# Performance work log

Hardware: AMD Instinct MI355X
Metric: run time of the kernel (lower is better)

The kernel has to match this reference:

```python
import jax, jax.numpy as jnp
import numpy as np
import math

B, S, D, H = 1, 2048, 4096, 32
HD = D // H  # 128
BASE = 10000.0
NEG = -1e9


def rotate_half(x):
    x1, x2 = x[..., : x.shape[-1] // 2], x[..., x.shape[-1] // 2 :]
    return jnp.concatenate((-x2, x1), axis=-1)


def setup_inputs() -> dict:
    key = jax.random.key(0)
    ks = jax.random.split(key, 5)
    scale = 1.0 / math.sqrt(D)
    hidden_states = jax.random.normal(ks[0], (B, S, D), dtype=jnp.float32)
    Wq = jax.random.normal(ks[1], (D, D), dtype=jnp.float32) * scale
    Wk = jax.random.normal(ks[2], (D, D), dtype=jnp.float32) * scale
    Wv = jax.random.normal(ks[3], (D, D), dtype=jnp.float32) * scale
    Wo = jax.random.normal(ks[4], (D, D), dtype=jnp.float32) * scale
    # causal additive mask [1,1,S,S]
    causal = jnp.tril(jnp.ones((S, S), dtype=bool))
    attention_mask = jnp.where(causal, 0.0, NEG).astype(jnp.float32)[None, None]
    # rotary cos/sin cache [1,1,S,HD]
    inv_freq = 1.0 / (BASE ** (jnp.arange(0, HD, 2, dtype=jnp.float32) / HD))
    freqs = jnp.arange(S, dtype=jnp.float32)[:, None] * inv_freq[None, :]
    emb = jnp.concatenate((freqs, freqs), axis=-1)
    cos = jnp.cos(emb)[None, None]
    sin = jnp.sin(emb)[None, None]
    return dict(hidden_states=hidden_states, attention_mask=attention_mask,
                cos=cos, sin=sin, Wq=Wq, Wk=Wk, Wv=Wv, Wo=Wo)


def reference(hidden_states, attention_mask, cos, sin, Wq, Wk, Wv, Wo):
    b, s, d = hidden_states.shape
    # projections (torch Linear: x @ W.T), reshape to [B,H,S,HD]
    def proj(W):
        return (hidden_states @ W.T).reshape(b, s, H, HD).transpose(0, 2, 1, 3)
    q, k, v = proj(Wq), proj(Wk), proj(Wv)
    # RoPE
    q = q * cos + rotate_half(q) * sin
    k = k * cos + rotate_half(k) * sin
    # scores [B,H,S,S], key pre-scaled as in original
    scores = jnp.einsum('bhqd,bhkd->bhqk', q, k / math.sqrt(HD)) + attention_mask
    attn = jax.nn.softmax(scores.astype(jnp.float32), axis=-1).astype(scores.dtype)
    out = jnp.einsum('bhqk,bhkd->bhqd', attn, v)
    out = out.transpose(0, 2, 1, 3).reshape(b, s, d)
    return out @ Wo.T
```

## Files before the change

### kernel.cpp

```cpp
#include <hip/hip_runtime.h>
#include <hip/hip_bf16.h>
#include <stdint.h>

#define DEV __device__ __forceinline__

typedef __bf16 bf16x8 __attribute__((ext_vector_type(8)));
typedef float f32x4 __attribute__((ext_vector_type(4)));
typedef unsigned short ushort8_t __attribute__((ext_vector_type(8)));
typedef unsigned short ushort4_t __attribute__((ext_vector_type(4)));

constexpr int S = 2048;
constexpr int D = 4096;
constexpr int H = 32;
constexpr int HD = 128;
constexpr float kSc = 0.08838834764831845f * 1.4426950408889634f;

DEV unsigned short f2bf(float f) {
    uint32_t u = __builtin_bit_cast(uint32_t, f);
    u += 0x7fffu + ((u >> 16) & 1u);
    return (unsigned short)(u >> 16);
}
DEV float bf2f(unsigned short h) {
    uint32_t u = ((uint32_t)h) << 16;
    return __builtin_bit_cast(float, u);
}

DEV void gload_lds16(const void* g, void* l) {
    __builtin_amdgcn_global_load_lds(
        (const __attribute__((address_space(1))) void*)g,
        (__attribute__((address_space(3))) void*)l,
        16, 0, 0);
}

DEV f32x4 mfma16(bf16x8 a, bf16x8 b, f32x4 c) {
    return __builtin_amdgcn_mfma_f32_16x16x32_bf16(a, b, c, 0, 0, 0);
}

__global__ __launch_bounds__(256) void cvt_all(const float* __restrict__ hs,
                                               const float* __restrict__ w0,
                                               const float* __restrict__ w1,
                                               const float* __restrict__ w2,
                                               const float* __restrict__ w3,
                                               unsigned short* __restrict__ hsb,
                                               unsigned short* __restrict__ o0,
                                               unsigned short* __restrict__ o1,
                                               unsigned short* __restrict__ o2,
                                               unsigned short* __restrict__ o3) {
    const int b = blockIdx.x;
    const float* in;
    unsigned short* out;
    size_t blk;
    if (b < 4096) {
        in = hs; out = hsb; blk = (size_t)b;
    } else {
        const int i = b - 4096;
        const int w = i >> 13;
        const int r = i & 8191;
        in  = (w == 0) ? w0 : (w == 1) ? w1 : (w == 2) ? w2 : w3;
        out = (w == 0) ? o0 : (w == 1) ? o1 : (w == 2) ? o2 : o3;
        blk = (size_t)r;
    }
    const size_t i8 = blk * 256 + threadIdx.x;
    f32x4 a = ((const f32x4*)in)[2 * i8];
    f32x4 c = ((const f32x4*)in)[2 * i8 + 1];
    ushort8_t o;
    o[0] = f2bf(a[0]); o[1] = f2bf(a[1]); o[2] = f2bf(a[2]); o[3] = f2bf(a[3]);
    o[4] = f2bf(c[0]); o[5] = f2bf(c[1]); o[6] = f2bf(c[2]); o[7] = f2bf(c[3]);
    ((ushort8_t*)out)[i8] = o;
}

__global__ __launch_bounds__(512, 2) void gemm_qkv8(const unsigned short* __restrict__ Ap,
                                                    const unsigned short* __restrict__ wq,
                                                    const unsigned short* __restrict__ wk,
                                                    const unsigned short* __restrict__ wv,
                                                    unsigned short* __restrict__ Qb,
                                                    unsigned short* __restrict__ Kb,
                                                    unsigned short* __restrict__ Vt) {
    extern __shared__ unsigned short lds8[];
    unsigned short (*As)[8192] = (unsigned short(*)[8192])lds8;
    unsigned short (*Bs)[8192] = (unsigned short(*)[8192])(lds8 + 32768);

    const int tix = threadIdx.x;
    const int lane = tix & 63;
    const int w = tix >> 6;
    const int g = (lane >> 4);
    const int rl = lane & 15;
    const int wm = w >> 2;
    const int wn = w & 3;
    const int bh = wn >> 1;
    const int bc0 = (wn & 1) * 64;
    const int rx = rl & 7;

    const int bid = blockIdx.x;
    const int wg = (bid & 7) * 48 + (bid >> 3);
    const int xx = wg % 48;
    const int yy = wg / 48;
    const int m0 = yy * 256;
    const int n0g = xx * 256;
    const int wsel = n0g >> 12;
    const int n0 = n0g & 4095;
    const unsigned short* Bp = (wsel == 0) ? wq : (wsel == 1) ? wk : wv;

    int srow[2], scol[2];
#pragma unroll
    for (int u = 0; u < 2; ++u) {
        const int c = u * 512 + tix;
        srow[u] = c >> 3;
        scol[u] = (((c & 7) ^ (srow[u] & 7)) << 3);
    }

    const char* aBase[2] = {(const char*)As[wm], (const char*)As[2 + wm]};
    const char* bBase[2] = {(const char*)Bs[bh], (const char*)Bs[2 + bh]};

    f32x4 acc[4][2][4] = {};
    bf16x8 bfr[4][2];

#define STG_A(kt, h, slot)                                                        \
    if ((kt) < 64) {                                                              \
        _Pragma("unroll") for (int u = 0; u < 2; ++u)                             \
            gload_lds16(Ap + (size_t)(m0 + (h) * 128 + srow[u]) * 4096 +          \
                            (kt) * 64 + scol[u],                                  \
                        &As[slot][(u * 512 + tix) * 8]);                          \
    }
#define STG_B(kt, h, slot)                                                        \
    if ((kt) < 64) {                                                              \
        _Pragma("unroll") for (int u = 0; u < 2; ++u)                             \
            gload_lds16(Bp + (size_t)(n0 + (h) * 128 + srow[u]) * 4096 +          \
                            (kt) * 64 + scol[u],                                  \
                        &Bs[slot][(u * 512 + tix) * 8]);                          \
    }

#define PHASE(pt, q, STG, VM)                                                     \
    {                                                                             \
        bf16x8 af[2][2];                                                          \
        _Pragma("unroll") for (int mi = 0; mi < 2; ++mi)                          \
        _Pragma("unroll") for (int ks = 0; ks < 2; ++ks) {                        \
            const int ab = ((q) * 32 + mi * 16 + rl) * 128 +                      \
                           ((((ks << 2) + g) ^ rx) << 4);                         \
            af[mi][ks] = *(const bf16x8*)(aBase[pt] + ab);                        \
        }                                                                         \
        if ((q) == 0) {                                                           \
            _Pragma("unroll") for (int nt = 0; nt < 4; ++nt)                      \
            _Pragma("unroll") for (int ks = 0; ks < 2; ++ks) {                    \
                const int bb = (bc0 + nt * 16 + rl) * 128 +                       \
                               ((((ks << 2) + g) ^ rx) << 4);                     \
                bfr[nt][ks] = *(const bf16x8*)(bBase[pt] + bb);                   \
            }                                                                     \
        }                                                                         \
        STG;                                                                      \
        if (VM) asm volatile("s_waitcnt vmcnt(4)" ::: "memory");                  \
        __builtin_amdgcn_s_barrier();                                             \
        __builtin_amdgcn_s_setprio(1);                                            \
        _Pragma("unroll") for (int ks = 0; ks < 2; ++ks)                          \
        _Pragma("unroll") for (int mi = 0; mi < 2; ++mi)                          \
        _Pragma("unroll") for (int nt = 0; nt < 4; ++nt)                          \
            acc[q][mi][nt] = mfma16(af[mi][ks], bfr[nt][ks], acc[q][mi][nt]);     \
        __builtin_amdgcn_s_setprio(0);                                            \
        __builtin_amdgcn_s_barrier();                                             \
    }

    STG_A(0, 0, 0); STG_A(0, 1, 1);
    STG_B(0, 0, 0); STG_B(0, 1, 1);
    STG_B(1, 0, 2); STG_B(1, 1, 3);
    __syncthreads();

    for (int i = 0; i < 32; ++i) {
        const int o = 2 * i + 1, ne = 2 * i + 2, no = 2 * i + 3;
        PHASE(0, 0, STG_A(o, 0, 2), 0)
        PHASE(0, 1, STG_A(o, 1, 3), 0)
        PHASE(0, 2, STG_B(ne, 0, 0), 0)
        PHASE(0, 3, STG_B(ne, 1, 1), 1)
        PHASE(1, 0, STG_A(ne, 0, 0), 0)
        PHASE(1, 1, STG_A(ne, 1, 1), 0)
        PHASE(1, 2, STG_B(no, 0, 2), 0)
        PHASE(1, 3, STG_B(no, 1, 3), 1)
    }
#undef PHASE
#undef STG_A
#undef STG_B

#pragma unroll
    for (int q = 0; q < 4; ++q)
#pragma unroll
        for (int mi = 0; mi < 2; ++mi)
#pragma unroll
            for (int nt = 0; nt < 4; ++nt) {
                const int row0 = m0 + wm * 128 + q * 32 + mi * 16 + g * 4;
                const int colg = n0 + wn * 64 + nt * 16 + rl;
                if (wsel == 2) {
                    ushort4_t v;
#pragma unroll
                    for (int r = 0; r < 4; ++r) v[r] = f2bf(acc[q][mi][nt][r]);
                    *(ushort4_t*)&Vt[(size_t)colg * S + row0] = v;
                } else {
                    unsigned short* o = (wsel == 0) ? Qb : Kb;
#pragma unroll
                    for (int r = 0; r < 4; ++r)
                        o[(size_t)(row0 + r) * 4096 + colg] = f2bf(acc[q][mi][nt][r]);
                }
            }
}

__global__ __launch_bounds__(256) void gemm_out(const unsigned short* __restrict__ A,
                                                const unsigned short* __restrict__ B,
                                                float* __restrict__ C) {
    __shared__ unsigned short As[128 * 64];
    __shared__ unsigned short Bs[128 * 64];
    const int t = threadIdx.x;
    const int lane = t & 63;
    const int wid = t >> 6;
    const int g = lane >> 4;
    const int rl = lane & 15;

    const int bid = blockIdx.x;
    const int wg = (bid & 7) * 64 + (bid >> 3);
    const int xx = wg % 32;
    const int yy = wg / 32;
    const int m0 = yy * 128;
    const int n0 = xx * 128;

    const int wm = (wid >> 1) * 64;
    const int wn = (wid & 1) * 64;
    constexpr int K = D, N = D;

    f32x4 acc[4][4] = {};

    for (int kt = 0; kt < K; kt += 64) {
#pragma unroll
        for (int r = 0; r < 4; ++r) {
            const int c = r * 256 + t;
            const int row = c >> 3;
            const int src = (c & 7) ^ (row & 7);
            const int dstChunk = r * 256 + wid * 64;
            gload_lds16(A + (size_t)(m0 + row) * K + kt + src * 8, &As[dstChunk * 8]);
            gload_lds16(B + (size_t)(n0 + row) * K + kt + src * 8, &Bs[dstChunk * 8]);
        }
        __syncthreads();
#pragma unroll
        for (int ks = 0; ks < 2; ++ks) {
            bf16x8 af[4], bfv[4];
#pragma unroll
            for (int i = 0; i < 4; ++i) {
                const int rowa = wm + i * 16 + rl;
                af[i] = *(const bf16x8*)&As[rowa * 64 + (((ks * 4 + g) ^ (rowa & 7)) << 3)];
                const int rowb = wn + i * 16 + rl;
                bfv[i] = *(const bf16x8*)&Bs[rowb * 64 + (((ks * 4 + g) ^ (rowb & 7)) << 3)];
            }
#pragma unroll
            for (int mi = 0; mi < 4; ++mi)
#pragma unroll
                for (int ni = 0; ni < 4; ++ni)
                    acc[mi][ni] = mfma16(af[mi], bfv[ni], acc[mi][ni]);
        }
        __syncthreads();
    }

#pragma unroll
    for (int mi = 0; mi < 4; ++mi) {
#pragma unroll
        for (int ni = 0; ni < 4; ++ni) {
            const int grow = m0 + wm + mi * 16 + g * 4;
            const int gcol = n0 + wn + ni * 16 + rl;
#pragma unroll
            for (int r = 0; r < 4; ++r)
                C[(size_t)(grow + r) * N + gcol] = acc[mi][ni][r];
        }
    }
}

__global__ __launch_bounds__(256) void rope_kernel(unsigned short* __restrict__ Qb,
                                                   unsigned short* __restrict__ Kb,
                                                   const float* __restrict__ cosT,
                                                   const float* __restrict__ sinT) {
    const int i = blockIdx.x * 256 + threadIdx.x;
    const int j8 = i & 7;
    const int h = (i >> 3) & 31;
    const int s = i >> 8;
    const size_t base = (size_t)s * D + h * HD + j8 * 8;
    const float* cp = cosT + s * HD + j8 * 8;
    const float* sp = sinT + s * HD + j8 * 8;
    float c1[8], s1[8], c2[8], s2[8];
#pragma unroll
    for (int k = 0; k < 8; ++k) { c1[k] = cp[k]; s1[k] = sp[k]; c2[k] = cp[k + 64]; s2[k] = sp[k + 64]; }

#pragma unroll
    for (int w = 0; w < 2; ++w) {
        unsigned short* p = (w == 0 ? Qb : Kb) + base;
        const float f = (w == 0) ? kSc : 1.0f;
        ushort8_t x1 = *(ushort8_t*)p;
        ushort8_t x2 = *(ushort8_t*)(p + 64);
        ushort8_t o1, o2;
#pragma unroll
        for (int k = 0; k < 8; ++k) {
            const float a = bf2f(x1[k]);
            const float b = bf2f(x2[k]);
            o1[k] = f2bf((a * c1[k] - b * s1[k]) * f);
            o2[k] = f2bf((b * c2[k] + a * s2[k]) * f);
        }
        *(ushort8_t*)p = o1;
        *(ushort8_t*)(p + 64) = o2;
    }
}

constexpr int NQT = S / 128;
__global__ __launch_bounds__(256, 2) void flash_attn(const unsigned short* __restrict__ Q,
                                                     const unsigned short* __restrict__ K,
                                                     const unsigned short* __restrict__ V,
                                                     unsigned short* __restrict__ O) {
    __shared__ unsigned short Ks[2][64 * 128];
    __shared__ unsigned short Vs[128 * 64];
    __shared__ unsigned short Ps[4][32 * 64];

    const int t = threadIdx.x;
    const int lane = t & 63;
    const int wid = t >> 6;
    const int g = lane >> 4;
    const int rl = lane & 15;
    const int bid = blockIdx.x;
    const int qt = (NQT - 1) - (bid >> 5);
    const int h = bid & 31;
    const int q0 = qt * 128;
    const int wrow0 = q0 + wid * 32;

    bf16x8 qf[2][4];
#pragma unroll
    for (int mi = 0; mi < 2; ++mi) {
        const unsigned short* qp = Q + (size_t)(wrow0 + mi * 16 + rl) * D + h * HD;
#pragma unroll
        for (int ks = 0; ks < 4; ++ks) qf[mi][ks] = *(const bf16x8*)(qp + ks * 32 + g * 8);
    }

    f32x4 accO[2][8] = {};
    float m2s[2] = {-1e30f, -1e30f};
    float lsum[2] = {0.f, 0.f};

#pragma unroll
    for (int r = 0; r < 4; ++r) {
        const int c = r * 256 + t;
        const int rowk = c >> 4;
        const int srck = (c & 15) ^ (rowk & 7);
        gload_lds16(K + (size_t)rowk * D + h * HD + srck * 8,
                    &Ks[0][(r * 256 + wid * 64) * 8]);
    }
    __syncthreads();

    int cur = 0;
    const int ntiles = 2 * qt + 2;
    for (int kv = 0; kv < ntiles; ++kv) {
        const int kv0 = kv * 64;
#pragma unroll
        for (int r = 0; r < 4; ++r) {
            const int c = r * 256 + t;
            const int rowv = c >> 3;
            const int srcv = (c & 7) ^ (rowv & 7);
            gload_lds16(V + (size_t)(h * HD + rowv) * S + kv0 + srcv * 8,
                        &Vs[(r * 256 + wid * 64) * 8]);
        }
        if (kv + 1 < ntiles) {
#pragma unroll
            for (int r = 0; r < 4; ++r) {
                const int c = r * 256 + t;
                const int rowk = c >> 4;
                const int srck = (c & 15) ^ (rowk & 7);
                gload_lds16(K + (size_t)(kv0 + 64 + rowk) * D + h * HD + srck * 8,
                            &Ks[cur ^ 1][(r * 256 + wid * 64) * 8]);
            }
        }

        const bool active = kv0 <= wrow0 + 31;
        if (active) {
            f32x4 sf[2][4];
#pragma unroll
            for (int mi = 0; mi < 2; ++mi)
#pragma unroll
                for (int nt = 0; nt < 4; ++nt) sf[mi][nt] = f32x4{0.f, 0.f, 0.f, 0.f};
            __builtin_amdgcn_s_setprio(1);
#pragma unroll
            for (int nt = 0; nt < 4; ++nt) {
                const int row = nt * 16 + rl;
#pragma unroll
                for (int ks = 0; ks < 4; ++ks) {
                    bf16x8 kf = *(const bf16x8*)&Ks[cur][row * 128 + (((ks * 4 + g) ^ (row & 7)) << 3)];
                    sf[0][nt] = mfma16(kf, qf[0][ks], sf[0][nt]);
                    sf[1][nt] = mfma16(kf, qf[1][ks], sf[1][nt]);
                }
            }
            __builtin_amdgcn_s_setprio(0);

            const bool needMask = (kv0 + 63 > wrow0);
            float cf2[2];
            bool chg = false;
#pragma unroll
            for (int mi = 0; mi < 2; ++mi) {
                const int qrow = wrow0 + mi * 16 + rl;
                float mx = -1e30f;
                if (needMask) {
#pragma unroll
                    for (int nt = 0; nt < 4; ++nt)
#pragma unroll
                        for (int r = 0; r < 4; ++r) {
                            const int kcol = kv0 + nt * 16 + g * 4 + r;
                            float s = sf[mi][nt][r];
                            s = (kcol > qrow) ? -1e30f : s;
                            sf[mi][nt][r] = s;
                            mx = fmaxf(mx, s);
                        }
                } else {
#pragma unroll
                    for (int nt = 0; nt < 4; ++nt)
#pragma unroll
                        for (int r = 0; r < 4; ++r) mx = fmaxf(mx, sf[mi][nt][r]);
                }
                mx = fmaxf(mx, __shfl_xor(mx, 16));
                mx = fmaxf(mx, __shfl_xor(mx, 32));
                const float mn = fmaxf(m2s[mi], mx);
                cf2[mi] = __builtin_amdgcn_exp2f(m2s[mi] - mn);
                chg |= (mn > m2s[mi]);
                m2s[mi] = mn;
                float rs = 0.f;
#pragma unroll
                for (int nt = 0; nt < 4; ++nt)
#pragma unroll
                    for (int r = 0; r < 4; ++r) {
                        const float p = __builtin_amdgcn_exp2f(sf[mi][nt][r] - mn);
                        sf[mi][nt][r] = p;
                        rs += p;
                    }
                rs += __shfl_xor(rs, 16);
                rs += __shfl_xor(rs, 32);
                lsum[mi] = lsum[mi] * cf2[mi] + rs;
            }

            if (__any((int)chg)) {
#pragma unroll
                for (int mi = 0; mi < 2; ++mi)
#pragma unroll
                    for (int nt = 0; nt < 8; ++nt)
#pragma unroll
                        for (int r = 0; r < 4; ++r) accO[mi][nt][r] *= cf2[mi];
            }

            unsigned short* myP = Ps[wid];
#pragma unroll
            for (int mi = 0; mi < 2; ++mi) {
                const int row = mi * 16 + rl;
                const int rxp = row & 7;
#pragma unroll
                for (int nt = 0; nt < 4; ++nt) {
                    ushort4_t v;
#pragma unroll
                    for (int r = 0; r < 4; ++r) v[r] = f2bf(sf[mi][nt][r]);
                    const int chunk = nt * 2 + (g >> 1);
                    *(ushort4_t*)&myP[row * 64 + ((chunk ^ rxp) << 3) + ((g & 1) << 2)] = v;
                }
            }
        }
        __syncthreads();

        if (active) {
            unsigned short* myP = Ps[wid];
            __builtin_amdgcn_s_setprio(1);
#pragma unroll
            for (int ks = 0; ks < 2; ++ks) {
                bf16x8 pa[2];
#pragma unroll
                for (int mi = 0; mi < 2; ++mi) {
                    const int row = mi * 16 + rl;
                    pa[mi] = *(const bf16x8*)&myP[row * 64 + (((ks * 4 + g) ^ (row & 7)) << 3)];
                }
#pragma unroll
                for (int nt = 0; nt < 8; ++nt) {
                    const int vrow = nt * 16 + rl;
                    bf16x8 vf = *(const bf16x8*)&Vs[vrow * 64 + (((ks * 4 + g) ^ (vrow & 7)) << 3)];
                    accO[0][nt] = mfma16(vf, pa[0], accO[0][nt]);
                    accO[1][nt] = mfma16(vf, pa[1], accO[1][nt]);
                }
            }
            __builtin_amdgcn_s_setprio(0);
        }
        __syncthreads();
        cur ^= 1;
    }

#pragma unroll
    for (int mi = 0; mi < 2; ++mi) {
        const float inv = 1.0f / lsum[mi];
        const int qrow = wrow0 + mi * 16 + rl;
#pragma unroll
        for (int nt = 0; nt < 8; ++nt) {
            ushort4_t v;
#pragma unroll
            for (int r = 0; r < 4; ++r) v[r] = f2bf(accO[mi][nt][r] * inv);
            *(ushort4_t*)&O[(size_t)qrow * D + h * HD + nt * 16 + g * 4] = v;
        }
    }
}

extern "C" void kernel_launch(void* const* d_in, const int* in_sizes, int n_in,
                              void* d_out, int out_size, void* d_ws, size_t ws_size,
                              hipStream_t stream) {
    const float* hs   = (const float*)d_in[0];
    const float* cosT = (const float*)d_in[2];
    const float* sinT = (const float*)d_in[3];
    const float* Wq   = (const float*)d_in[4];
    const float* Wk   = (const float*)d_in[5];
    const float* Wv   = (const float*)d_in[6];
    const float* Wo   = (const float*)d_in[7];

    char* ws = (char*)d_ws;
    const size_t MB = 1ull << 20;
    unsigned short* hsb = (unsigned short*)(ws);
    unsigned short* wqb = (unsigned short*)(ws + 16 * MB);
    unsigned short* wkb = (unsigned short*)(ws + 48 * MB);
    unsigned short* wvb = (unsigned short*)(ws + 80 * MB);
    unsigned short* wob = (unsigned short*)(ws + 112 * MB);
    unsigned short* Qb  = (unsigned short*)(ws + 144 * MB);
    unsigned short* Kb  = (unsigned short*)(ws + 160 * MB);
    unsigned short* Vt  = (unsigned short*)(ws + 176 * MB);
    unsigned short* AOb = (unsigned short*)(ws + 192 * MB);

    cvt_all<<<4096 + 4 * 8192, 256, 0, stream>>>(hs, Wq, Wk, Wv, Wo,
                                                 hsb, wqb, wkb, wvb, wob);

    gemm_qkv8<<<384, 512, 131072, stream>>>(hsb, wqb, wkb, wvb, Qb, Kb, Vt);

    rope_kernel<<<2048, 256, 0, stream>>>(Qb, Kb, cosT, sinT);

    flash_attn<<<dim3(NQT * H), 256, 0, stream>>>(Qb, Kb, Vt, AOb);

    gemm_out<<<512, 256, 0, stream>>>(AOb, wob, (float*)d_out);
}
```

Before: 465.6 us.

## Generalize pipelined GEMM over tile width; use it for QKV and output projections

The QKV GEMM becomes a template with a configurable N-tile width. It runs with 192-wide tiles over the three contiguous weight buffers, giving 512 blocks instead of 384 so the work divides evenly across the CUs. The simple single-buffered output-projection GEMM is replaced by the same multi-stage pipelined kernel with 256x128 tiles and fp32 output. Wait counts are adjusted to match the new per-thread load counts, with a full drain on the last iteration. The QKV path now assumes the Wq, Wk and Wv bf16 buffers sit back to back in the workspace.

Measured after the change: 417.8 us. -10.3%, faster.

```diff
diff --git a/kernel.cpp b/kernel.cpp
--- a/kernel.cpp
+++ b/kernel.cpp
@@ -69,68 +69,73 @@
     ((ushort8_t*)out)[i8] = o;
 }
 
-__global__ __launch_bounds__(512, 2) void gemm_qkv8(const unsigned short* __restrict__ Ap,
-                                                    const unsigned short* __restrict__ wq,
-                                                    const unsigned short* __restrict__ wk,
-                                                    const unsigned short* __restrict__ wv,
-                                                    unsigned short* __restrict__ Qb,
-                                                    unsigned short* __restrict__ Kb,
-                                                    unsigned short* __restrict__ Vt) {
+template <int BN, int OMODE>
+__global__ __launch_bounds__(512, 2) void gemm8(const unsigned short* __restrict__ Ap,
+                                                const unsigned short* __restrict__ Bp,
+                                                unsigned short* __restrict__ Oq,
+                                                unsigned short* __restrict__ Ok,
+                                                unsigned short* __restrict__ Ovt,
+                                                float* __restrict__ Of) {
+    constexpr int NT = BN / 64;
+    constexpr int NB = BN / 64;
     extern __shared__ unsigned short lds8[];
     unsigned short (*As)[8192] = (unsigned short(*)[8192])lds8;
-    unsigned short (*Bs)[8192] = (unsigned short(*)[8192])(lds8 + 32768);
+    unsigned short* Bs0 = lds8 + 4 * 8192;
+    unsigned short* Bs1 = Bs0 + BN * 64;
 
     const int tix = threadIdx.x;
     const int lane = tix & 63;
     const int w = tix >> 6;
-    const int g = (lane >> 4);
+    const int g = lane >> 4;
     const int rl = lane & 15;
     const int wm = w >> 2;
     const int wn = w & 3;
-    const int bh = wn >> 1;
-    const int bc0 = (wn & 1) * 64;
+    const int bc0 = wn * (BN / 4);
     const int rx = rl & 7;
 
-    const int bid = blockIdx.x;
-    const int wg = (bid & 7) * 48 + (bid >> 3);
-    const int xx = wg % 48;
-    const int yy = wg / 48;
+    const int yy = blockIdx.x & 7;
+    const int xx = blockIdx.x >> 3;
     const int m0 = yy * 256;
-    const int n0g = xx * 256;
-    const int wsel = n0g >> 12;
-    const int n0 = n0g & 4095;
-    const unsigned short* Bp = (wsel == 0) ? wq : (wsel == 1) ? wk : wv;
-
-    int srow[2], scol[2];
+    const int n0 = xx * BN;
+
+    int srowA[2], scolA[2];
 #pragma unroll
     for (int u = 0; u < 2; ++u) {
         const int c = u * 512 + tix;
-        srow[u] = c >> 3;
-        scol[u] = (((c & 7) ^ (srow[u] & 7)) << 3);
+        srowA[u] = c >> 3;
+        scolA[u] = ((c & 7) ^ (srowA[u] & 7)) << 3;
+    }
+    int srowB[NB], scolB[NB];
+#pragma unroll
+    for (int u = 0; u < NB; ++u) {
+        const int c = u * 512 + tix;
+        srowB[u] = c >> 3;
+        scolB[u] = ((c & 7) ^ (srowB[u] & 7)) << 3;
     }
 
     const char* aBase[2] = {(const char*)As[wm], (const char*)As[2 + wm]};
-    const char* bBase[2] = {(const char*)Bs[bh], (const char*)Bs[2 + bh]};
-
-    f32x4 acc[4][2][4] = {};
-    bf16x8 bfr[4][2];
-
-#define STG_A(kt, h, slot)                                                        \
-    if ((kt) < 64) {                                                              \
+    const char* bBase[2] = {(const char*)Bs0, (const char*)Bs1};
+
+    f32x4 acc[4][2][NT] = {};
+    bf16x8 bfr[NT][2];
+
+#define STG_A8(t, h, slot)                                                        \
+    if ((t) < 64) {                                                               \
         _Pragma("unroll") for (int u = 0; u < 2; ++u)                             \
-            gload_lds16(Ap + (size_t)(m0 + (h) * 128 + srow[u]) * 4096 +          \
-                            (kt) * 64 + scol[u],                                  \
+            gload_lds16(Ap + (size_t)(m0 + (h) * 128 + srowA[u]) * 4096 +         \
+                            (t) * 64 + scolA[u],                                  \
                         &As[slot][(u * 512 + tix) * 8]);                          \
     }
-#define STG_B(kt, h, slot)                                                        \
-    if ((kt) < 64) {                                                              \
-        _Pragma("unroll") for (int u = 0; u < 2; ++u)                             \
-            gload_lds16(Bp + (size_t)(n0 + (h) * 128 + srow[u]) * 4096 +          \
-                            (kt) * 64 + scol[u],                                  \
-                        &Bs[slot][(u * 512 + tix) * 8]);                          \
-    }
-
-#define PHASE(pt, q, STG, VM)                                                     \
+#define STG_B8(t, slot)                                                           \
+    if ((t) < 64) {                                                               \
+        unsigned short* bs_ = (slot) ? Bs1 : Bs0;                                 \
+        _Pragma("unroll") for (int u = 0; u < NB; ++u)                            \
+            gload_lds16(Bp + (size_t)(n0 + srowB[u]) * 4096 +                     \
+                            (t) * 64 + scolB[u],                                  \
+                        &bs_[(u * 512 + tix) * 8]);                               \
+    }
+
+#define PHASE8(pt, q, STG, VM)                                                    \
     {                                                                             \
         bf16x8 af[2][2];                                                          \
         _Pragma("unroll") for (int mi = 0; mi < 2; ++mi)                          \
@@ -140,7 +145,7 @@
             af[mi][ks] = *(const bf16x8*)(aBase[pt] + ab);                        \
         }                                                                         \
         if ((q) == 0) {                                                           \
-            _Pragma("unroll") for (int nt = 0; nt < 4; ++nt)                      \
+            _Pragma("unroll") for (int nt = 0; nt < NT; ++nt)                     \
             _Pragma("unroll") for (int ks = 0; ks < 2; ++ks) {                    \
                 const int bb = (bc0 + nt * 16 + rl) * 128 +                       \
                                ((((ks << 2) + g) ^ rx) << 4);                     \
@@ -148,124 +153,73 @@
             }                                                                     \
         }                                                                         \
         STG;                                                                      \
-        if (VM) asm volatile("s_waitcnt vmcnt(4)" ::: "memory");                  \
+        if (VM) {                                                                 \
+            if (last) {                                                           \
+                asm volatile("s_waitcnt vmcnt(0)" ::: "memory");                  \
+            } else if constexpr (NB == 3) {                                       \
+                asm volatile("s_waitcnt vmcnt(3)" ::: "memory");                  \
+            } else {                                                              \
+                asm volatile("s_waitcnt vmcnt(2)" ::: "memory");                  \
+            }                                                                     \
+        }                                                                         \
         __builtin_amdgcn_s_barrier();                                             \
         __builtin_amdgcn_s_setprio(1);                                            \
         _Pragma("unroll") for (int ks = 0; ks < 2; ++ks)                          \
         _Pragma("unroll") for (int mi = 0; mi < 2; ++mi)                          \
-        _Pragma("unroll") for (int nt = 0; nt < 4; ++nt)                          \
+        _Pragma("unroll") for (int nt = 0; nt < NT; ++nt)                         \
             acc[q][mi][nt] = mfma16(af[mi][ks], bfr[nt][ks], acc[q][mi][nt]);     \
         __builtin_amdgcn_s_setprio(0);                                            \
         __builtin_amdgcn_s_barrier();                                             \
     }
 
-    STG_A(0, 0, 0); STG_A(0, 1, 1);
-    STG_B(0, 0, 0); STG_B(0, 1, 1);
-    STG_B(1, 0, 2); STG_B(1, 1, 3);
+    STG_A8(0, 0, 0); STG_A8(0, 1, 1);
+    STG_B8(0, 0); STG_B8(1, 1);
     __syncthreads();
 
     for (int i = 0; i < 32; ++i) {
+        const bool last = (i == 31);
         const int o = 2 * i + 1, ne = 2 * i + 2, no = 2 * i + 3;
-        PHASE(0, 0, STG_A(o, 0, 2), 0)
-        PHASE(0, 1, STG_A(o, 1, 3), 0)
-        PHASE(0, 2, STG_B(ne, 0, 0), 0)
-        PHASE(0, 3, STG_B(ne, 1, 1), 1)
-        PHASE(1, 0, STG_A(ne, 0, 0), 0)
-        PHASE(1, 1, STG_A(ne, 1, 1), 0)
-        PHASE(1, 2, STG_B(no, 0, 2), 0)
-        PHASE(1, 3, STG_B(no, 1, 3), 1)
-    }
-#undef PHASE
-#undef STG_A
-#undef STG_B
+        PHASE8(0, 0, STG_A8(o, 0, 2), 0)
+        PHASE8(0, 1, STG_A8(o, 1, 3), 0)
+        PHASE8(0, 2, STG_B8(ne, 0), 0)
+        PHASE8(0, 3, ((void)0), 1)
+        PHASE8(1, 0, STG_A8(ne, 0, 0), 0)
+        PHASE8(1, 1, STG_A8(ne, 1, 1), 0)
+        PHASE8(1, 2, STG_B8(no, 1), 0)
+        PHASE8(1, 3, ((void)0), 1)
+    }
+#undef PHASE8
+#undef STG_A8
+#undef STG_B8
 
 #pragma unroll
     for (int q = 0; q < 4; ++q)
 #pragma unroll
         for (int mi = 0; mi < 2; ++mi)
 #pragma unroll
-            for (int nt = 0; nt < 4; ++nt) {
+            for (int nt = 0; nt < NT; ++nt) {
                 const int row0 = m0 + wm * 128 + q * 32 + mi * 16 + g * 4;
-                const int colg = n0 + wn * 64 + nt * 16 + rl;
-                if (wsel == 2) {
-                    ushort4_t v;
-#pragma unroll
-                    for (int r = 0; r < 4; ++r) v[r] = f2bf(acc[q][mi][nt][r]);
-                    *(ushort4_t*)&Vt[(size_t)colg * S + row0] = v;
+                const int gc = n0 + bc0 + nt * 16 + rl;
+                if constexpr (OMODE == 0) {
+                    const int sel = gc >> 12;
+                    const int col = gc & 4095;
+                    if (sel == 2) {
+                        ushort4_t v;
+#pragma unroll
+                        for (int r = 0; r < 4; ++r) v[r] = f2bf(acc[q][mi][nt][r]);
+                        *(ushort4_t*)&Ovt[(size_t)col * S + row0] = v;
+                    } else {
+                        unsigned short* op = sel ? Ok : Oq;
+#pragma unroll
+                        for (int r = 0; r < 4; ++r)
+                            op[(size_t)(row0 + r) * 4096 + col] = f2bf(acc[q][mi][nt][r]);
+                    }
                 } else {
-                    unsigned short* o = (wsel == 0) ? Qb : Kb;
 #pragma unroll
                     for (int r = 0; r < 4; ++r)
-                        o[(size_t)(row0 + r) * 4096 + colg] = f2bf(acc[q][mi][nt][r]);
-                }
-            }
-}
-
-__global__ __launch_bounds__(256) void gemm_out(const unsigned short* __restrict__ A,
-                                                const unsigned short* __restrict__ B,
-                                                float* __restrict__ C) {
-    __shared__ unsigned short As[128 * 64];
-    __shared__ unsigned short Bs[128 * 64];
-    const int t = threadIdx.x;
-    const int lane = t & 63;
-    const int wid = t >> 6;
-    const int g = lane >> 4;
-    const int rl = lane & 15;
-
-    const int bid = blockIdx.x;
-    const int wg = (bid & 7) * 64 + (bid >> 3);
-    const int xx = wg % 32;
-    const int yy = wg / 32;
-    const int m0 = yy * 128;
-    const int n0 = xx * 128;
-
-    const int wm = (wid >> 1) * 64;
-    const int wn = (wid & 1) * 64;
-    constexpr int K = D, N = D;
-
-    f32x4 acc[4][4] = {};
-
-    for (int kt = 0; kt < K; kt += 64) {
-#pragma unroll
-        for (int r = 0; r < 4; ++r) {
-            const int c = r * 256 + t;
-            const int row = c >> 3;
-            const int src = (c & 7) ^ (row & 7);
-            const int dstChunk = r * 256 + wid * 64;
-            gload_lds16(A + (size_t)(m0 + row) * K + kt + src * 8, &As[dstChunk * 8]);
-            gload_lds16(B + (size_t)(n0 + row) * K + kt + src * 8, &Bs[dstChunk * 8]);
-        }
-        __syncthreads();
-#pragma unroll
-        for (int ks = 0; ks < 2; ++ks) {
-            bf16x8 af[4], bfv[4];
-#pragma unroll
-            for (int i = 0; i < 4; ++i) {
-                const int rowa = wm + i * 16 + rl;
-                af[i] = *(const bf16x8*)&As[rowa * 64 + (((ks * 4 + g) ^ (rowa & 7)) << 3)];
-                const int rowb = wn + i * 16 + rl;
-                bfv[i] = *(const bf16x8*)&Bs[rowb * 64 + (((ks * 4 + g) ^ (rowb & 7)) << 3)];
-            }
-#pragma unroll
-            for (int mi = 0; mi < 4; ++mi)
-#pragma unroll
-                for (int ni = 0; ni < 4; ++ni)
-                    acc[mi][ni] = mfma16(af[mi], bfv[ni], acc[mi][ni]);
-        }
-        __syncthreads();
-    }
-
-#pragma unroll
-    for (int mi = 0; mi < 4; ++mi) {
-#pragma unroll
-        for (int ni = 0; ni < 4; ++ni) {
-            const int grow = m0 + wm + mi * 16 + g * 4;
-            const int gcol = n0 + wn + ni * 16 + rl;
-#pragma unroll
-            for (int r = 0; r < 4; ++r)
-                C[(size_t)(grow + r) * N + gcol] = acc[mi][ni][r];
-        }
-    }
+                        Of[(size_t)(row0 + r) * 4096 + gc] = acc[q][mi][nt][r];
+                }
+            }
 }
 
 __global__ __launch_bounds__(256) void rope_kernel(unsigned short* __restrict__ Qb,
@@ -522,11 +476,12 @@
     cvt_all<<<4096 + 4 * 8192, 256, 0, stream>>>(hs, Wq, Wk, Wv, Wo,
                                                  hsb, wqb, wkb, wvb, wob);
 
-    gemm_qkv8<<<384, 512, 131072, stream>>>(hsb, wqb, wkb, wvb, Qb, Kb, Vt);
+    gemm8<192, 0><<<512, 512, 114688, stream>>>(hsb, wqb, Qb, Kb, Vt, nullptr);
 
     rope_kernel<<<2048, 256, 0, stream>>>(Qb, Kb, cosT, sinT);
 
     flash_attn<<<dim3(NQT * H), 256, 0, stream>>>(Qb, Kb, Vt, AOb);
 
-    gemm_out<<<512, 256, 0, stream>>>(AOb, wob, (float*)d_out);
-}
+    gemm8<128, 1><<<256, 512, 98304, stream>>>(AOb, wob, nullptr, nullptr, nullptr,
+                                               (float*)d_out);
+}
```
